# Performance work log

Hardware: AMD Instinct MI355X
Metric: run time of the kernel (lower is better)

Reference implementation:

```python
import jax, jax.numpy as jnp
import numpy as np

K_SYNAPSES = 32          # numberOfSynapsesPerSegment
THETA = 16               # segment activation threshold (k/2 of the +/-1 synapses)


def _make_weight(key, n_neurons, prev_size, k):
    """Dense int8-style EISANI weight: exactly k synapses per neuron, values +/-1, rest 0.
    Mirrors _initialise_layer_weights (non-EI, dense, static-connection branch)."""
    k1, k2 = jax.random.split(key)
    scores = jax.random.uniform(k1, (n_neurons, prev_size))
    _, idx = jax.lax.top_k(scores, k)  # k distinct random columns per neuron
    signs = jnp.where(jax.random.bernoulli(k2, 0.5, (n_neurons, k)), 1.0, -1.0)
    w = jnp.zeros((n_neurons, prev_size), jnp.float32)
    return w.at[jnp.arange(n_neurons)[:, None], idx].set(signs)


def setup_inputs() -> dict:
    key = jax.random.key(0)
    ks = jax.random.split(key, 5)
    B, F, H, C, L = 1024, 4096, 4096, 10, 3  # batch, encodedFeatureSize, hidden, classes, hidden layers
    # binary encoded tabular input (continuous-var thermometer/gray encoding -> {0,1})
    x = (jax.random.uniform(ks[0], (B, F)) > 0.5).astype(jnp.float32)
    w0 = _make_weight(ks[1], H, F, K_SYNAPSES)
    w1 = _make_weight(ks[2], H, H, K_SYNAPSES)
    w2 = _make_weight(ks[3], H, H, K_SYNAPSES)
    out_conn = jax.random.normal(ks[4], (L, H, C), jnp.float32) * 0.02
    return {"x": x, "w0": w0, "w1": w1, "w2": w2, "out_conn": out_conn}


def reference(x, w0, w1, w2, out_conn):
    # Hidden pass: signed binary connection matmul + threshold activation per layer.
    a = x  # [B, F] in {0,1}
    acts = []
    for w in (w0, w1, w2):
        z = a @ w.T                                   # [B, H] integer-valued dot of {0,1} with {-1,0,+1}
        a = (z >= THETA).astype(jnp.float32)          # segment fires if enough synapses active
        acts.append(a)
    acts = jnp.stack(acts)                            # [L, B, H]
    # Output layer: every hidden layer projects to the class scores.
    return jnp.einsum('lbh,lhc->bc', acts, out_conn)  # [B, C]
```

## Files before the change

### kernel.cpp

```cpp
#include <hip/hip_runtime.h>
#include <stdint.h>


__global__ __launch_bounds__(256) void sparsify_kernel(const float* __restrict__ w0,
                                                       const float* __restrict__ w1,
                                                       const float* __restrict__ w2,
                                                       uint32_t* __restrict__ syn) {
    const int wid   = blockIdx.x * 4 + (threadIdx.x >> 6);
    const int lane  = threadIdx.x & 63;
    const int layer = wid >> 12;
    const int r     = wid & 4095;
    const float* wp = (layer == 0 ? w0 : (layer == 1 ? w1 : w2)) + (size_t)r * 4096;
    const float4* wp4 = (const float4*)wp;
    uint32_t* srow  = syn + (size_t)wid * 32;
    const uint64_t lt = (1ull << lane) - 1ull;
    uint32_t base = 0;
    for (int grp = 0; grp < 4; ++grp) {
        float4 v[4];
#pragma unroll
        for (int it = 0; it < 4; ++it)
            v[it] = wp4[grp * 256 + it * 64 + lane];
#pragma unroll
        for (int it = 0; it < 4; ++it) {
            const int col = grp * 1024 + it * 256 + lane * 4;
            const float4 q = v[it];
            const uint64_t m0 = __ballot(q.x != 0.0f);
            const uint64_t m1 = __ballot(q.y != 0.0f);
            const uint64_t m2 = __ballot(q.z != 0.0f);
            const uint64_t m3 = __ballot(q.w != 0.0f);
            const uint32_t t0 = (uint32_t)__popcll(m0), t1 = (uint32_t)__popcll(m1);
            const uint32_t t2 = (uint32_t)__popcll(m2), t3 = (uint32_t)__popcll(m3);
            if (q.x != 0.0f) { const uint32_t s = base + (uint32_t)__popcll(m0 & lt);
                if (s < 32u) srow[s] = (uint32_t)col | (q.x < 0.0f ? 0x80000000u : 0u); }
            if (q.y != 0.0f) { const uint32_t s = base + t0 + (uint32_t)__popcll(m1 & lt);
                if (s < 32u) srow[s] = (uint32_t)(col + 1) | (q.y < 0.0f ? 0x80000000u : 0u); }
            if (q.z != 0.0f) { const uint32_t s = base + t0 + t1 + (uint32_t)__popcll(m2 & lt);
                if (s < 32u) srow[s] = (uint32_t)(col + 2) | (q.z < 0.0f ? 0x80000000u : 0u); }
            if (q.w != 0.0f) { const uint32_t s = base + t0 + t1 + t2 + (uint32_t)__popcll(m3 & lt);
                if (s < 32u) srow[s] = (uint32_t)(col + 3) | (q.w < 0.0f ? 0x80000000u : 0u); }
            base += t0 + t1 + t2 + t3;
        }
    }
}

__global__ __launch_bounds__(256) void pack_kernel(const float* __restrict__ x,
                                                   uint64_t* __restrict__ bits) {
    const int c  = blockIdx.x * 256 + threadIdx.x;
    const int bg = blockIdx.y;
    const float* xp = x + (size_t)bg * 64 * 4096 + c;
    uint64_t acc = 0;
#pragma unroll
    for (int r = 0; r < 64; ++r) {
        const float v = xp[(size_t)r * 4096];
        acc |= (uint64_t)(v > 0.5f) << r;
    }
    bits[(size_t)bg * 4096 + c] = acc;
}

__global__ __launch_bounds__(256) void layer_kernel(const uint64_t* __restrict__ in_bits,
                                                    const uint32_t* __restrict__ syn,
                                                    uint64_t* __restrict__ out_bits) {
    __shared__ uint64_t lb[4096];
    const int tid = threadIdx.x;
    const int bg  = blockIdx.y;
    const uint64_t* src = in_bits + (size_t)bg * 4096;
#pragma unroll
    for (int i = 0; i < 8; ++i)
        ((uint4*)lb)[i * 256 + tid] = ((const uint4*)src)[i * 256 + tid];
    __syncthreads();

    const int h = blockIdx.x * 256 + tid;
    const uint32_t* srow = syn + (size_t)h * 32;
    uint32_t sw[32];
#pragma unroll
    for (int k = 0; k < 8; ++k)
        *(uint4*)(sw + k * 4) = *(const uint4*)(srow + k * 4);

    uint32_t thr = 16;
#pragma unroll
    for (int k = 0; k < 32; ++k) thr += sw[k] >> 31;

    uint64_t a0 = 0, a1 = 0, a2 = 0, a3 = 0, a4 = 0;
    uint64_t b0 = 0, b1 = 0, b2 = 0, b3 = 0, b4 = 0;
#pragma unroll
    for (int k = 0; k < 32; k += 2) {
        {
            const uint32_t s = sw[k];
            uint64_t c = lb[s & 4095] ^ (uint64_t)(int64_t)((int32_t)s >> 31);
            uint64_t t;
            t = a0 & c; a0 ^= c; c = t;
            t = a1 & c; a1 ^= c; c = t;
            t = a2 & c; a2 ^= c; c = t;
            t = a3 & c; a3 ^= c; c = t;
            a4 ^= c;
        }
        {
            const uint32_t s = sw[k + 1];
            uint64_t c = lb[s & 4095] ^ (uint64_t)(int64_t)((int32_t)s >> 31);
            uint64_t t;
            t = b0 & c; b0 ^= c; c = t;
            t = b1 & c; b1 ^= c; c = t;
            t = b2 & c; b2 ^= c; c = t;
            t = b3 & c; b3 ^= c; c = t;
            b4 ^= c;
        }
    }
    uint64_t c;
    const uint64_t v0 = a0 ^ b0;     c = a0 & b0;
    const uint64_t v1 = a1 ^ b1 ^ c; c = (a1 & b1) | (c & (a1 ^ b1));
    const uint64_t v2 = a2 ^ b2 ^ c; c = (a2 & b2) | (c & (a2 ^ b2));
    const uint64_t v3 = a3 ^ b3 ^ c; c = (a3 & b3) | (c & (a3 ^ b3));
    const uint64_t v4 = a4 ^ b4 ^ c; c = (a4 & b4) | (c & (a4 ^ b4));
    const uint64_t v5 = c;
    uint64_t gt = 0, eq = ~0ull;
    {
        uint64_t tb;
        tb = ((thr >> 5) & 1u) ? ~0ull : 0ull; gt |= eq & v5 & ~tb; eq &= ~(v5 ^ tb);
        tb = ((thr >> 4) & 1u) ? ~0ull : 0ull; gt |= eq & v4 & ~tb; eq &= ~(v4 ^ tb);
        tb = ((thr >> 3) & 1u) ? ~0ull : 0ull; gt |= eq & v3 & ~tb; eq &= ~(v3 ^ tb);
        tb = ((thr >> 2) & 1u) ? ~0ull : 0ull; gt |= eq & v2 & ~tb; eq &= ~(v2 ^ tb);
        tb = ((thr >> 1) & 1u) ? ~0ull : 0ull; gt |= eq & v1 & ~tb; eq &= ~(v1 ^ tb);
        tb = ((thr >> 0) & 1u) ? ~0ull : 0ull; gt |= eq & v0 & ~tb; eq &= ~(v0 ^ tb);
    }
    out_bits[(size_t)bg * 4096 + h] = gt | eq;
}

__global__ __launch_bounds__(256) void outA_kernel(const uint64_t* __restrict__ bits,
                                                   const float* __restrict__ oc,
                                                   float* __restrict__ partial) {
    __shared__ float red[4][640];
    const int tid   = threadIdx.x;
    const int chunk = blockIdx.x;
    const int bg    = blockIdx.y;
    const int wave  = tid >> 6;
    const int lane  = tid & 63;
    const int r0 = chunk * 256 + wave * 64;
    const int l  = r0 >> 12;
    const int h0 = r0 & 4095;
    const uint64_t* bw = bits + (size_t)l * 65536 + (size_t)bg * 4096 + h0;
    const float* op = oc + (size_t)r0 * 10;

    float acc[10];
#pragma unroll
    for (int cc = 0; cc < 10; ++cc) acc[cc] = 0.0f;

#pragma unroll 4
    for (int i = 0; i < 64; ++i) {
        const uint64_t w = bw[i];
        const float bitf = (float)((w >> lane) & 1ull);
        const float2* o2 = (const float2*)(op + (size_t)i * 10);
        const float2 p0 = o2[0], p1 = o2[1], p2 = o2[2], p3 = o2[3], p4 = o2[4];
        acc[0] += bitf * p0.x; acc[1] += bitf * p0.y;
        acc[2] += bitf * p1.x; acc[3] += bitf * p1.y;
        acc[4] += bitf * p2.x; acc[5] += bitf * p2.y;
        acc[6] += bitf * p3.x; acc[7] += bitf * p3.y;
        acc[8] += bitf * p4.x; acc[9] += bitf * p4.y;
    }
#pragma unroll
    for (int cc = 0; cc < 10; ++cc) red[wave][lane * 10 + cc] = acc[cc];
    __syncthreads();

    float* dst = partial + ((size_t)bg * 48 + chunk) * 640;
    for (int idx = tid; idx < 640; idx += 256)
        dst[idx] = red[0][idx] + red[1][idx] + red[2][idx] + red[3][idx];
}

__global__ __launch_bounds__(256) void outB_kernel(const float* __restrict__ partial,
                                                   float* __restrict__ out) {
    const int g  = blockIdx.x * 256 + threadIdx.x;
    const int bg = g / 640;
    const int s  = g - bg * 640;
    const float* p = partial + (size_t)bg * 48 * 640 + s;
    float sum = 0.0f;
#pragma unroll
    for (int ch = 0; ch < 48; ++ch) sum += p[ch * 640];
    out[g] = sum;
}

extern "C" void kernel_launch(void* const* d_in, const int* in_sizes, int n_in,
                              void* d_out, int out_size, void* d_ws, size_t ws_size,
                              hipStream_t stream) {
    const float* x  = (const float*)d_in[0];
    const float* w0 = (const float*)d_in[1];
    const float* w1 = (const float*)d_in[2];
    const float* w2 = (const float*)d_in[3];
    const float* oc = (const float*)d_in[4];
    float* out = (float*)d_out;

    uint32_t* syn    = (uint32_t*)d_ws;
    float*    part   = (float*)d_ws;
    uint64_t* bitsx  = (uint64_t*)((char*)d_ws + 2097152);
    uint64_t* bits0  = bitsx + 65536;
    uint64_t* bits1  = bits0 + 65536;
    uint64_t* bits2  = bits1 + 65536;

    sparsify_kernel<<<3072, 256, 0, stream>>>(w0, w1, w2, syn);
    pack_kernel<<<dim3(16, 16), 256, 0, stream>>>(x, bitsx);

    layer_kernel<<<dim3(16, 16), 256, 0, stream>>>(bitsx, syn,          bits0);
    layer_kernel<<<dim3(16, 16), 256, 0, stream>>>(bits0, syn + 131072, bits1);
    layer_kernel<<<dim3(16, 16), 256, 0, stream>>>(bits1, syn + 262144, bits2);

    outA_kernel<<<dim3(48, 16), 256, 0, stream>>>(bits0, oc, part);
    outB_kernel<<<40, 256, 0, stream>>>(part, out);
}
```

Before: 250.3 us.

## Merge weight sparsify and input pack into one prep kernel with LDS loads

Combines the weight-sparsification and input bit-packing kernels into one launch. Each weight row is now handled by a full 256-thread block that loads the row through global_load_lds into shared memory, with a cross-wave prefix count, instead of one wave per row. Packing now uses float4 loads across 16 rows per wave and merges four 16-bit pieces through LDS. The aims are to remove a launch, raise memory parallelism on the 200 MB weight read, and widen the x loads, at the cost of an extra barrier and LDS staging per row.

```diff
diff --git a/kernel.cpp b/kernel.cpp
--- a/kernel.cpp
+++ b/kernel.cpp
@@ -1,60 +1,104 @@
 #include <hip/hip_runtime.h>
 #include <stdint.h>
 
-
-__global__ __launch_bounds__(256) void sparsify_kernel(const float* __restrict__ w0,
-                                                       const float* __restrict__ w1,
-                                                       const float* __restrict__ w2,
-                                                       uint32_t* __restrict__ syn) {
-    const int wid   = blockIdx.x * 4 + (threadIdx.x >> 6);
-    const int lane  = threadIdx.x & 63;
-    const int layer = wid >> 12;
-    const int r     = wid & 4095;
-    const float* wp = (layer == 0 ? w0 : (layer == 1 ? w1 : w2)) + (size_t)r * 4096;
-    const float4* wp4 = (const float4*)wp;
-    uint32_t* srow  = syn + (size_t)wid * 32;
-    const uint64_t lt = (1ull << lane) - 1ull;
-    uint32_t base = 0;
-    for (int grp = 0; grp < 4; ++grp) {
-        float4 v[4];
+#define AS1 __attribute__((address_space(1)))
+#define AS3 __attribute__((address_space(3)))
+
+
+__global__ __launch_bounds__(256) void prep_kernel(const float* __restrict__ x,
+                                                   const float* __restrict__ w0,
+                                                   const float* __restrict__ w1,
+                                                   const float* __restrict__ w2,
+                                                   uint32_t* __restrict__ syn,
+                                                   uint64_t* __restrict__ bits) {
+    __shared__ __align__(16) uint8_t smem[16448];
+    const int blk  = blockIdx.x;
+    const int tid  = threadIdx.x;
+    const int wave = tid >> 6;
+    const int lane = tid & 63;
+
+    if (blk < 12288) {
+        float*    lb   = (float*)smem;
+        uint32_t* wcnt = (uint32_t*)(smem + 16384);
+        const int layer = blk >> 12;
+        const int r     = blk & 4095;
+        const float* wp = (layer == 0 ? w0 : (layer == 1 ? w1 : w2)) + (size_t)r * 4096;
+        uint32_t* srow  = syn + (size_t)blk * 32;
+
+#pragma unroll
+        for (int i = 0; i < 4; ++i) {
+            const int c = wave * 4 + i;
+            __builtin_amdgcn_global_load_lds(
+                (const AS1 void*)(wp + c * 256 + lane * 4),
+                (AS3 void*)(lb + c * 256), 16, 0, 0);
+        }
+        __syncthreads();
+
+        float4 q[4];
 #pragma unroll
         for (int it = 0; it < 4; ++it)
-            v[it] = wp4[grp * 256 + it * 64 + lane];
+            q[it] = ((const float4*)lb)[wave * 256 + it * 64 + lane];
+        uint32_t cnt = 0;
 #pragma unroll
         for (int it = 0; it < 4; ++it) {
-            const int col = grp * 1024 + it * 256 + lane * 4;
-            const float4 q = v[it];
-            const uint64_t m0 = __ballot(q.x != 0.0f);
-            const uint64_t m1 = __ballot(q.y != 0.0f);
-            const uint64_t m2 = __ballot(q.z != 0.0f);
-            const uint64_t m3 = __ballot(q.w != 0.0f);
+            cnt += (uint32_t)__popcll(__ballot(q[it].x != 0.0f));
+            cnt += (uint32_t)__popcll(__ballot(q[it].y != 0.0f));
+            cnt += (uint32_t)__popcll(__ballot(q[it].z != 0.0f));
+            cnt += (uint32_t)__popcll(__ballot(q[it].w != 0.0f));
+        }
+        if (lane == 0) wcnt[wave] = cnt;
+        __syncthreads();
+        uint32_t base = 0;
+#pragma unroll
+        for (int w2 = 0; w2 < 4; ++w2) base += (w2 < wave) ? wcnt[w2] : 0u;
+
+        const uint64_t lt = (1ull << lane) - 1ull;
+#pragma unroll
+        for (int it = 0; it < 4; ++it) {
+            const int col = wave * 1024 + it * 256 + lane * 4;
+            const float4 p = q[it];
+            const uint64_t m0 = __ballot(p.x != 0.0f);
+            const uint64_t m1 = __ballot(p.y != 0.0f);
+            const uint64_t m2 = __ballot(p.z != 0.0f);
+            const uint64_t m3 = __ballot(p.w != 0.0f);
             const uint32_t t0 = (uint32_t)__popcll(m0), t1 = (uint32_t)__popcll(m1);
             const uint32_t t2 = (uint32_t)__popcll(m2), t3 = (uint32_t)__popcll(m3);
-            if (q.x != 0.0f) { const uint32_t s = base + (uint32_t)__popcll(m0 & lt);
-                if (s < 32u) srow[s] = (uint32_t)col | (q.x < 0.0f ? 0x80000000u : 0u); }
-            if (q.y != 0.0f) { const uint32_t s = base + t0 + (uint32_t)__popcll(m1 & lt);
-                if (s < 32u) srow[s] = (uint32_t)(col + 1) | (q.y < 0.0f ? 0x80000000u : 0u); }
-            if (q.z != 0.0f) { const uint32_t s = base + t0 + t1 + (uint32_t)__popcll(m2 & lt);
-                if (s < 32u) srow[s] = (uint32_t)(col + 2) | (q.z < 0.0f ? 0x80000000u : 0u); }
-            if (q.w != 0.0f) { const uint32_t s = base + t0 + t1 + t2 + (uint32_t)__popcll(m3 & lt);
-                if (s < 32u) srow[s] = (uint32_t)(col + 3) | (q.w < 0.0f ? 0x80000000u : 0u); }
+            if (p.x != 0.0f) { const uint32_t s = base + (uint32_t)__popcll(m0 & lt);
+                if (s < 32u) srow[s] = (uint32_t)col | (p.x < 0.0f ? 0x80000000u : 0u); }
+            if (p.y != 0.0f) { const uint32_t s = base + t0 + (uint32_t)__popcll(m1 & lt);
+                if (s < 32u) srow[s] = (uint32_t)(col + 1) | (p.y < 0.0f ? 0x80000000u : 0u); }
+            if (p.z != 0.0f) { const uint32_t s = base + t0 + t1 + (uint32_t)__popcll(m2 & lt);
+                if (s < 32u) srow[s] = (uint32_t)(col + 2) | (p.z < 0.0f ? 0x80000000u : 0u); }
+            if (p.w != 0.0f) { const uint32_t s = base + t0 + t1 + t2 + (uint32_t)__popcll(m3 & lt);
+                if (s < 32u) srow[s] = (uint32_t)(col + 3) | (p.w < 0.0f ? 0x80000000u : 0u); }
             base += t0 + t1 + t2 + t3;
         }
-    }
-}
-
-__global__ __launch_bounds__(256) void pack_kernel(const float* __restrict__ x,
-                                                   uint64_t* __restrict__ bits) {
-    const int c  = blockIdx.x * 256 + threadIdx.x;
-    const int bg = blockIdx.y;
-    const float* xp = x + (size_t)bg * 64 * 4096 + c;
-    uint64_t acc = 0;
-#pragma unroll
-    for (int r = 0; r < 64; ++r) {
-        const float v = xp[(size_t)r * 4096];
-        acc |= (uint64_t)(v > 0.5f) << r;
-    }
-    bits[(size_t)bg * 4096 + c] = acc;
+    } else {
+        uint16_t* pk = (uint16_t*)smem;
+        const int blk2   = blk - 12288;
+        const int bg     = blk2 >> 4;
+        const int cchunk = blk2 & 15;
+        const float* xb = x + ((size_t)(bg * 64 + wave * 16)) * 4096 + cchunk * 256 + lane * 4;
+        uint32_t b0 = 0, b1 = 0, b2 = 0, b3 = 0;
+#pragma unroll
+        for (int r = 0; r < 16; ++r) {
+            const float4 p = *(const float4*)(xb + (size_t)r * 4096);
+            b0 |= (uint32_t)(p.x > 0.5f) << r;
+            b1 |= (uint32_t)(p.y > 0.5f) << r;
+            b2 |= (uint32_t)(p.z > 0.5f) << r;
+            b3 |= (uint32_t)(p.w > 0.5f) << r;
+        }
+        pk[wave * 256 + lane * 4 + 0] = (uint16_t)b0;
+        pk[wave * 256 + lane * 4 + 1] = (uint16_t)b1;
+        pk[wave * 256 + lane * 4 + 2] = (uint16_t)b2;
+        pk[wave * 256 + lane * 4 + 3] = (uint16_t)b3;
+        __syncthreads();
+        const uint64_t vv = (uint64_t)pk[tid]
+                          | ((uint64_t)pk[256 + tid] << 16)
+                          | ((uint64_t)pk[512 + tid] << 32)
+                          | ((uint64_t)pk[768 + tid] << 48);
+        bits[(size_t)bg * 4096 + cchunk * 256 + tid] = vv;
+    }
 }
 
 __global__ __launch_bounds__(256) void layer_kernel(const uint64_t* __restrict__ in_bits,
@@ -194,8 +238,7 @@
     uint64_t* bits1  = bits0 + 65536;
     uint64_t* bits2  = bits1 + 65536;
 
-    sparsify_kernel<<<3072, 256, 0, stream>>>(w0, w1, w2, syn);
-    pack_kernel<<<dim3(16, 16), 256, 0, stream>>>(x, bitsx);
+    prep_kernel<<<12544, 256, 0, stream>>>(x, w0, w1, w2, syn, bitsx);
 
     layer_kernel<<<dim3(16, 16), 256, 0, stream>>>(bitsx, syn,          bits0);
     layer_kernel<<<dim3(16, 16), 256, 0, stream>>>(bits0, syn + 131072, bits1);
```

After: 237.5 us. 5.1% less time.
